# Kernel tuning notes

Measured on AMD Instinct MI355X. Metric: run time of the kernel, lower is better.

Reference implementation:

```python
import jax, jax.numpy as jnp
import numpy as np

N_NODES = 50000
N_EDGES = 800000
HEADS = 5
NFEAT = 5
C1 = 32  # hidden_layers


def setup_inputs() -> dict:
    key = jax.random.key(0)
    ks = jax.random.split(key, 20)
    s = 0.3  # glorot-ish scale
    d = {
        "x": jax.random.normal(ks[0], (N_NODES, NFEAT), jnp.float32),
        "edge_attr": jax.random.uniform(ks[1], (N_EDGES, 1), jnp.float32),
        "src": jax.random.randint(ks[2], (N_EDGES,), 0, N_NODES, jnp.int32),
        "dst": jax.random.randint(ks[3], (N_EDGES,), 0, N_NODES, jnp.int32),
        # conv1: in=5 -> heads=5, out=32, concat
        "W1": jax.random.normal(ks[4], (NFEAT, HEADS * C1), jnp.float32) * s,
        "a_src1": jax.random.normal(ks[5], (HEADS, C1), jnp.float32) * s,
        "a_dst1": jax.random.normal(ks[6], (HEADS, C1), jnp.float32) * s,
        "We1": jax.random.normal(ks[7], (1, HEADS * C1), jnp.float32) * s,
        "ae1": jax.random.normal(ks[8], (HEADS, C1), jnp.float32) * s,
        "b1": jnp.zeros((HEADS * C1,), jnp.float32),
        # conv2: in=160 -> heads=5, out=1, mean over heads
        "W2": jax.random.normal(ks[9], (HEADS * C1, HEADS * 1), jnp.float32) * 0.08,
        "a_src2": jax.random.normal(ks[10], (HEADS, 1), jnp.float32) * s,
        "a_dst2": jax.random.normal(ks[11], (HEADS, 1), jnp.float32) * s,
        "We2": jax.random.normal(ks[12], (1, HEADS * 1), jnp.float32) * s,
        "ae2": jax.random.normal(ks[13], (HEADS, 1), jnp.float32) * s,
        "b2": jnp.zeros((1,), jnp.float32),
        "Wlin": jax.random.normal(ks[14], (1, 1), jnp.float32),
    }
    return d


def gat_layer(x, src, dst, eattr, W, a_src, a_dst, We, a_e, bias, concat, n_nodes):
    """PyG GATConv with edge_dim, self-loops already added by caller."""
    H, C = a_src.shape
    h = (x @ W).reshape(-1, H, C)                      # [N,H,C]
    alpha_s = (h * a_src[None]).sum(-1)                # [N,H]
    alpha_d = (h * a_dst[None]).sum(-1)                # [N,H]
    ee = (eattr @ We).reshape(-1, H, C)                # [E,H,C]
    alpha_e = (ee * a_e[None]).sum(-1)                 # [E,H]
    logits = jax.nn.leaky_relu(alpha_s[src] + alpha_d[dst] + alpha_e, 0.2)
    # segment softmax over destination nodes
    m = jax.ops.segment_max(logits, dst, num_segments=n_nodes)
    m = jnp.where(jnp.isfinite(m), m, 0.0)
    ex = jnp.exp(logits - m[dst])
    denom = jax.ops.segment_sum(ex, dst, num_segments=n_nodes)
    alpha = ex / (denom[dst] + 1e-16)                  # [E,H]
    msg = (alpha[:, :, None] * h[src]).reshape(-1, H * C)
    agg = jax.ops.segment_sum(msg, dst, num_segments=n_nodes).reshape(n_nodes, H, C)
    if concat:
        return agg.reshape(n_nodes, H * C) + bias
    return agg.mean(axis=1) + bias


def reference(x, edge_attr, src, dst, W1, a_src1, a_dst1, We1, ae1, b1,
              W2, a_src2, a_dst2, We2, ae2, b2, Wlin):
    n = x.shape[0]
    loop = jnp.arange(n, dtype=src.dtype)
    s = jnp.concatenate([src, loop])
    t = jnp.concatenate([dst, loop])
    # self-loop edge_attr = mean of edge_attr (PyG fill_value='mean')
    ea_loop = jnp.broadcast_to(edge_attr.mean(axis=0, keepdims=True), (n, edge_attr.shape[1]))
    ea = jnp.concatenate([edge_attr, ea_loop], axis=0)

    x1 = gat_layer(x, s, t, ea, W1, a_src1, a_dst1, We1, ae1, b1, True, n)
    x2 = jax.nn.relu(x1)
    # dropout p=0.2 is identity in eval mode
    x4 = gat_layer(x2, s, t, ea, W2, a_src2, a_dst2, We2, ae2, b2, False, n)
    x5 = x4 @ Wlin                                     # Linear(1,1,bias=False)
    return jax.nn.sigmoid(x5)                          # [N,1]
```

## Files before the change

### kernel.cpp

```cpp
#include <hip/hip_runtime.h>
#include <hip/hip_fp16.h>
#include <math.h>

#define N_NODES 50000
#define N_EDGES 800000
#define E2 (N_EDGES + N_NODES)
#define HEADS 5
#define C1 32
#define F1 160

#define BSZ 64
#define NBK 782
#define NBL 128
#define CH  6641
#define MTOT (NBK*NBL)
#define MC  391
#define GRID_H1 (N_NODES/4)
#define CAP 1408

#define AGG1_NPB 32
#define AGG1_NB  1563

static constexpr size_t alignup(size_t x){ return (x + 255) & ~size_t(255); }
static constexpr size_t OFF_SCAL  = 0;
static constexpr size_t OFF_H     = alignup(OFF_SCAL + 64*4);
static constexpr size_t OFF_EAS   = alignup(OFF_H    + (size_t)MTOT*4);
static constexpr size_t OFF_PART  = alignup(OFF_EAS  + (size_t)NBL*4);
static constexpr size_t OFF_PPREF = alignup(OFF_PART + (size_t)MC*4);
static constexpr size_t OFF_BST   = alignup(OFF_PPREF+ (size_t)MC*4);
static constexpr size_t OFF_OFFS  = alignup(OFF_BST  + (size_t)(NBK+1)*4);
static constexpr size_t OFF_BPACK = alignup(OFF_OFFS + (size_t)(N_NODES+1)*4);
static constexpr size_t OFF_EDG   = alignup(OFF_BPACK+ (size_t)E2*8);
static constexpr size_t OFF_AS16  = alignup(OFF_EDG  + (size_t)E2*4);
static constexpr size_t OFF_AD16  = alignup(OFF_AS16 + (size_t)N_NODES*8*2);
static constexpr size_t OFF_G16   = alignup(OFF_AD16 + (size_t)N_NODES*8*2);
static constexpr size_t OFF_AD2P  = alignup(OFF_G16  + (size_t)N_NODES*16*2);
static constexpr size_t OFF_H1Q   = alignup(OFF_AD2P + (size_t)N_NODES*8*4);
static constexpr size_t OFF_X2H   = alignup(OFF_H1Q  + (size_t)N_NODES*F1);
static constexpr size_t OFF_P2    = alignup(OFF_X2H  + (size_t)N_NODES*F1*2);

typedef float vf2 __attribute__((ext_vector_type(2)));
__device__ __forceinline__ float4 fp8x4_to_f32(unsigned int r){
  vf2 lo = __builtin_amdgcn_cvt_pk_f32_fp8((int)r, false);
  vf2 hi = __builtin_amdgcn_cvt_pk_f32_fp8((int)r, true);
  return make_float4(lo.x, lo.y, hi.x, hi.y);
}

__global__ __launch_bounds__(320) void k_init(const float* __restrict__ x, const float* __restrict__ W1,
                       const float* __restrict__ as1w, const float* __restrict__ ad1w,
                       unsigned short* __restrict__ h1qh, __half* __restrict__ as16, __half* __restrict__ ad16,
                       const int* __restrict__ dst, const float* __restrict__ ea,
                       int* __restrict__ H, float* __restrict__ easum){
  __shared__ float sW[5*F1];
  int t = threadIdx.x;
  if (blockIdx.x < GRID_H1){
    for (int k = t; k < 5*F1; k += 320) sW[k] = W1[k];
    __syncthreads();
    int nl = t / 80;
    int c  = t - nl*80;
    int n  = blockIdx.x*4 + nl;
    int c0 = 2*c;
    float hv0 = 0.f, hv1 = 0.f;
    #pragma unroll
    for (int f = 0; f < 5; f++){
      float xv = x[n*5 + f];
      hv0 += xv * sW[f*F1 + c0];
      hv1 += xv * sW[f*F1 + c0 + 1];
    }
    int pk = __builtin_amdgcn_cvt_pk_fp8_f32(hv0, hv1, 0, false);
    int hh = c >> 4, pp = c & 15;
    h1qh[(size_t)hh*(N_NODES*16) + n*16 + pp] = (unsigned short)(pk & 0xFFFF);
    float vs = hv0*as1w[c0] + hv1*as1w[c0+1];
    float vd = hv0*ad1w[c0] + hv1*ad1w[c0+1];
    #pragma unroll
    for (int m = 8; m >= 1; m >>= 1){
      vs += __shfl_xor(vs, m, 64);
      vd += __shfl_xor(vd, m, 64);
    }
    if ((c & 15) == 0){
      int h = c >> 4;
      as16[n*8 + h] = __float2half(vs);
      ad16[n*8 + h] = __float2half(vd);
    }
  } else {
    int* hist = (int*)sW;
    float* wsum = (float*)&hist[NBK + 1];
    for (int k = t; k < NBK; k += 320) hist[k] = 0;
    __syncthreads();
    int b = blockIdx.x - GRID_H1;
    int e0 = b*CH, e1 = min(e0 + CH, E2);
    float s = 0.f;
    for (int e = e0 + t; e < e1; e += 320){
      int d;
      if (e < N_EDGES){ d = dst[e]; s += ea[e]; }
      else d = e - N_EDGES;
      atomicAdd(&hist[d >> 6], 1);
    }
    #pragma unroll
    for (int m = 1; m < 64; m <<= 1) s += __shfl_xor(s, m, 64);
    if ((t & 63) == 0) wsum[t >> 6] = s;
    __syncthreads();
    for (int k = t; k < NBK; k += 320) H[(size_t)k*NBL + b] = hist[k];
    if (t == 0) easum[b] = wsum[0] + wsum[1] + wsum[2] + wsum[3] + wsum[4];
  }
}

__global__ void k_s1(const int* __restrict__ H, int* __restrict__ partial){
  int i = blockIdx.x*256 + threadIdx.x;
  int v = (i < MTOT) ? H[i] : 0;
  #pragma unroll
  for (int m = 1; m < 64; m <<= 1) v += __shfl_xor(v, m, 64);
  __shared__ int sh[4];
  if ((threadIdx.x & 63) == 0) sh[threadIdx.x >> 6] = v;
  __syncthreads();
  if (threadIdx.x == 0) partial[blockIdx.x] = sh[0] + sh[1] + sh[2] + sh[3];
}

__global__ __launch_bounds__(512) void k_s2p(const int* __restrict__ partial, int* __restrict__ ppref,
                      int* __restrict__ offs, int* __restrict__ bstart,
                      const float* __restrict__ easum,
                      const float* __restrict__ We1, const float* __restrict__ ae1,
                      const float* __restrict__ We2, const float* __restrict__ ae2,
                      float* __restrict__ scal){
  __shared__ int sp[512];
  __shared__ float sh_ea[NBL];
  int t = threadIdx.x;
  if (t < NBL) sh_ea[t] = easum[t];
  if (t >= 448 && t < 448 + HEADS){
    int h = t - 448;
    float s = 0.f;
    for (int c = 0; c < C1; c++) s += We1[h*C1 + c] * ae1[h*C1 + c];
    scal[2 + h] = s;
    scal[7 + h] = We2[h] * ae2[h];
  }
  int v = (t < MC) ? partial[t] : 0;
  sp[t] = v;
  __syncthreads();
  if (t == 511){
    float es = 0.f;
    for (int i = 0; i < NBL; i++) es += sh_ea[i];
    scal[1] = es / (float)N_EDGES;
  }
  for (int off = 1; off < 512; off <<= 1){
    int u = (t >= off) ? sp[t - off] : 0;
    __syncthreads();
    sp[t] += u;
    __syncthreads();
  }
  if (t < MC) ppref[t] = sp[t] - v;
  if (t == 0){ offs[N_NODES] = E2; bstart[NBK] = E2; }
}

__global__ void k_s3(int* __restrict__ H, const int* __restrict__ ppref, int* __restrict__ bstart){
  __shared__ int sp[256];
  int b = blockIdx.x, t = threadIdx.x;
  int i = b*256 + t;
  int v = (i < MTOT) ? H[i] : 0;
  sp[t] = v;
  __syncthreads();
  for (int off = 1; off < 256; off <<= 1){
    int u = (t >= off) ? sp[t - off] : 0;
    __syncthreads();
    sp[t] += u;
    __syncthreads();
  }
  int P = ppref[b] + sp[t] - v;
  if (i < MTOT){
    H[i] = P;
    if (i % NBL == 0) bstart[i / NBL] = P;
  }
}

__global__ __launch_bounds__(256) void k_scat(const int* __restrict__ src, const int* __restrict__ dst,
                       const float* __restrict__ ea, const float* __restrict__ scal,
                       const int* __restrict__ H, int2* __restrict__ bpack){
  __shared__ int lofs[NBK];
  int b = blockIdx.x;
  for (int k = threadIdx.x; k < NBK; k += 256) lofs[k] = H[(size_t)k*NBL + b];
  __syncthreads();
  float mean = scal[1];
  int e0 = b*CH, e1 = min(e0 + CH, E2);
  for (int e = e0 + threadIdx.x; e < e1; e += 256){
    int d, s; float a;
    if (e < N_EDGES){ d = dst[e]; s = src[e]; a = ea[e]; }
    else { d = s = e - N_EDGES; a = mean; }
    int pos = atomicAdd(&lofs[d >> 6], 1);
    bpack[pos] = make_int2(s | ((d & 63) << 16), __float_as_int(a));
  }
}

__global__ __launch_bounds__(256) void k_final2(const int* __restrict__ bstart,
                        const int2* __restrict__ bpack,
                        int* __restrict__ offs, unsigned int* __restrict__ edge2){
  __shared__ int cnt[BSZ], cur[BSZ];
  __shared__ unsigned int s_edge[CAP];
  int k = blockIdx.x, t = threadIdx.x;
  int base = k*BSZ;
  if (t < BSZ) cnt[t] = 0;
  __syncthreads();
  int r0 = bstart[k], r1 = bstart[k + 1];
  int sz = r1 - r0;
  for (int j = r0 + t; j < r1; j += 256) atomicAdd(&cnt[(bpack[j].x >> 16) & 63], 1);
  __syncthreads();
  if (t == 0){
    int run = 0;
    for (int i = 0; i < BSZ; i++){ int c = cnt[i]; cnt[i] = run; cur[i] = run; run += c; }
  }
  __syncthreads();
  if (t < BSZ){
    int n = base + t;
    if (n < N_NODES) offs[n] = r0 + cnt[t];
  }
  if (sz <= CAP){
    for (int j = r0 + t; j < r1; j += 256){
      int2 v = bpack[j];
      int lp = atomicAdd(&cur[(v.x >> 16) & 63], 1);
      s_edge[lp] = (unsigned int)(v.x & 0xFFFF) |
                   ((unsigned int)__half_as_ushort(__float2half(__int_as_float(v.y))) << 16);
    }
    __syncthreads();
    for (int i = t; i < sz; i += 256) edge2[r0 + i] = s_edge[i];
  } else {
    for (int j = r0 + t; j < r1; j += 256){
      int2 v = bpack[j];
      int pos = r0 + atomicAdd(&cur[(v.x >> 16) & 63], 1);
      edge2[pos] = (unsigned int)(v.x & 0xFFFF) |
                   ((unsigned int)__half_as_ushort(__float2half(__int_as_float(v.y))) << 16);
    }
  }
}

__global__ __launch_bounds__(256) void k_logit(const int* __restrict__ offs,
                      const unsigned int* __restrict__ edge2,
                      const __half* __restrict__ as16, const __half* __restrict__ ad16,
                      const float* __restrict__ scal,
                      unsigned int* __restrict__ P01, unsigned int* __restrict__ P2){
  int gl = threadIdx.x >> 3;
  int q  = threadIdx.x & 7;
  int n  = blockIdx.x*AGG1_NPB + gl;
  if (n >= N_NODES) return;
  union { uint4 u; __half2 h[4]; } AD; AD.u = *(const uint4*)(ad16 + (size_t)n*8);
  float ad0 = __low2float(AD.h[0]), ad1 = __high2float(AD.h[0]);
  float ad2 = __low2float(AD.h[1]), ad3 = __high2float(AD.h[1]);
  float ad4 = __low2float(AD.h[2]);
  float wd0 = scal[2], wd1 = scal[3], wd2 = scal[4], wd3 = scal[5], wd4 = scal[6];
  int j0 = offs[n], j1 = offs[n + 1];
  for (int j = j0 + q; j < j1; j += 8){
    unsigned int e = edge2[j];
    unsigned int lo = e & 0xFFFFu;
    int s = (int)lo;
    float c = __half2float(__ushort_as_half((unsigned short)(e >> 16)));
    union { uint4 u; __half2 h[4]; } AS; AS.u = *(const uint4*)(as16 + (size_t)s*8);
    float l0 = __low2float(AS.h[0])  + ad0 + c*wd0;  l0 = fminf(fmaxf(l0, 0.2f*l0), 10.f);
    float l1 = __high2float(AS.h[0]) + ad1 + c*wd1;  l1 = fminf(fmaxf(l1, 0.2f*l1), 10.f);
    float l2 = __low2float(AS.h[1])  + ad2 + c*wd2;  l2 = fminf(fmaxf(l2, 0.2f*l2), 10.f);
    float l3 = __high2float(AS.h[1]) + ad3 + c*wd3;  l3 = fminf(fmaxf(l3, 0.2f*l3), 10.f);
    float l4 = __low2float(AS.h[2])  + ad4 + c*wd4;  l4 = fminf(fmaxf(l4, 0.2f*l4), 10.f);
    unsigned int p0 = (unsigned int)__half_as_ushort(__float2half(__expf(l0)));
    unsigned int p1 = (unsigned int)__half_as_ushort(__float2half(__expf(l1)));
    unsigned int p2 = (unsigned int)__half_as_ushort(__float2half(__expf(l2)));
    unsigned int p3 = (unsigned int)__half_as_ushort(__float2half(__expf(l3)));
    unsigned int p4 = (unsigned int)__half_as_ushort(__float2half(__expf(l4)));
    P01[j]                  = lo | (p0 << 16);
    P01[(size_t)E2 + j]     = lo | (p1 << 16);
    P2[j]                   = lo | (p2 << 16);
    P2[(size_t)E2 + j]      = lo | (p3 << 16);
    P2[(size_t)2*E2 + j]    = lo | (p4 << 16);
  }
}

__global__ __launch_bounds__(256) void k_agg1(const int* __restrict__ offs,
                      const unsigned int* __restrict__ P01, const unsigned int* __restrict__ P2,
                      const unsigned short* __restrict__ h1qh,
                      const float* __restrict__ b1, __half* __restrict__ x2h){
  int head = blockIdx.x / AGG1_NB;
  int nb   = blockIdx.x - head*AGG1_NB;
  int gl   = threadIdx.x >> 3;
  int q    = threadIdx.x & 7;
  int n    = nb*AGG1_NPB + gl;
  if (n >= N_NODES) return;
  const unsigned int* EP = (head < 2) ? (P01 + (size_t)head*E2)
                                      : (P2  + (size_t)(head-2)*E2);
  const unsigned int* h1row = (const unsigned int*)h1qh + (size_t)head*(N_NODES*8) + q;
  int j0 = offs[n], j1 = offs[n + 1];
  float a0 = 0.f, a1 = 0.f, a2 = 0.f, a3 = 0.f, den = 0.f;
  int j = j0;
  for (; j + 7 < j1; j += 8){
    uint4 sa = *(const uint4*)(EP + j);
    uint4 sb = *(const uint4*)(EP + j + 4);
    unsigned int e0 = sa.x, e1 = sa.y, e2v = sa.z, e3 = sa.w;
    unsigned int e4 = sb.x, e5 = sb.y, e6 = sb.z, e7 = sb.w;
    int s0 = e0 & 0xFFFF, s1 = e1 & 0xFFFF, s2 = e2v & 0xFFFF, s3 = e3 & 0xFFFF;
    int s4 = e4 & 0xFFFF, s5 = e5 & 0xFFFF, s6 = e6 & 0xFFFF, s7 = e7 & 0xFFFF;
    unsigned int r0 = h1row[s0*8];
    unsigned int r1 = h1row[s1*8];
    unsigned int r2 = h1row[s2*8];
    unsigned int r3 = h1row[s3*8];
    unsigned int r4 = h1row[s4*8];
    unsigned int r5 = h1row[s5*8];
    unsigned int r6 = h1row[s6*8];
    unsigned int r7 = h1row[s7*8];
    float p0 = __half2float(__ushort_as_half((unsigned short)(e0 >> 16)));
    float p1 = __half2float(__ushort_as_half((unsigned short)(e1 >> 16)));
    float p2 = __half2float(__ushort_as_half((unsigned short)(e2v >> 16)));
    float p3 = __half2float(__ushort_as_half((unsigned short)(e3 >> 16)));
    float p4 = __half2float(__ushort_as_half((unsigned short)(e4 >> 16)));
    float p5 = __half2float(__ushort_as_half((unsigned short)(e5 >> 16)));
    float p6 = __half2float(__ushort_as_half((unsigned short)(e6 >> 16)));
    float p7 = __half2float(__ushort_as_half((unsigned short)(e7 >> 16)));
    den += ((p0 + p1) + (p2 + p3)) + ((p4 + p5) + (p6 + p7));
    float4 f0 = fp8x4_to_f32(r0), f1 = fp8x4_to_f32(r1);
    float4 f2 = fp8x4_to_f32(r2), f3 = fp8x4_to_f32(r3);
    float4 f4 = fp8x4_to_f32(r4), f5 = fp8x4_to_f32(r5);
    float4 f6 = fp8x4_to_f32(r6), f7 = fp8x4_to_f32(r7);
    a0 += p0*f0.x; a1 += p0*f0.y; a2 += p0*f0.z; a3 += p0*f0.w;
    a0 += p1*f1.x; a1 += p1*f1.y; a2 += p1*f1.z; a3 += p1*f1.w;
    a0 += p2*f2.x; a1 += p2*f2.y; a2 += p2*f2.z; a3 += p2*f2.w;
    a0 += p3*f3.x; a1 += p3*f3.y; a2 += p3*f3.z; a3 += p3*f3.w;
    a0 += p4*f4.x; a1 += p4*f4.y; a2 += p4*f4.z; a3 += p4*f4.w;
    a0 += p5*f5.x; a1 += p5*f5.y; a2 += p5*f5.z; a3 += p5*f5.w;
    a0 += p6*f6.x; a1 += p6*f6.y; a2 += p6*f6.z; a3 += p6*f6.w;
    a0 += p7*f7.x; a1 += p7*f7.y; a2 += p7*f7.z; a3 += p7*f7.w;
  }
  for (; j < j1; ++j){
    unsigned int e = EP[j];
    int s = e & 0xFFFF;
    float p = __half2float(__ushort_as_half((unsigned short)(e >> 16)));
    den += p;
    float4 f = fp8x4_to_f32(h1row[s*8]);
    a0 += p*f.x; a1 += p*f.y; a2 += p*f.z; a3 += p*f.w;
  }
  float inv = 1.f / (den + 1e-16f);
  float4 bb = *(const float4*)(b1 + head*C1 + 4*q);
  float v0 = fmaxf(a0*inv + bb.x, 0.f);
  float v1 = fmaxf(a1*inv + bb.y, 0.f);
  float v2 = fmaxf(a2*inv + bb.z, 0.f);
  float v3 = fmaxf(a3*inv + bb.w, 0.f);
  __half2 o0 = __floats2half2_rn(v0, v1);
  __half2 o1 = __floats2half2_rn(v2, v3);
  *(uint2*)(x2h + (size_t)n*F1 + head*C1 + 4*q) =
      make_uint2(*(unsigned int*)&o0, *(unsigned int*)&o1);
}

__global__ __launch_bounds__(256) void k_h2(const __half* __restrict__ x2h, const float* __restrict__ W2,
                    const float* __restrict__ asw2, const float* __restrict__ adw2,
                    __half* __restrict__ G16, float* __restrict__ ad2p){
  __shared__ float sW[F1*HEADS];
  for (int k = threadIdx.x; k < F1*HEADS; k += 256) sW[k] = W2[k];
  __syncthreads();
  int w = threadIdx.x >> 6, l = threadIdx.x & 63;
  int n = blockIdx.x*4 + w;
  const __half2* x22 = (const __half2*)x2h;
  float acc[HEADS] = {0.f, 0.f, 0.f, 0.f, 0.f};
  for (int k2 = l; k2 < 80; k2 += 64){
    float2 f = __half22float2(x22[(size_t)n*80 + k2]);
    #pragma unroll
    for (int h = 0; h < HEADS; h++)
      acc[h] += f.x * sW[(2*k2)*HEADS + h] + f.y * sW[(2*k2+1)*HEADS + h];
  }
  #pragma unroll
  for (int m = 1; m < 64; m <<= 1){
    #pragma unroll
    for (int h = 0; h < HEADS; h++) acc[h] += __shfl_xor(acc[h], m, 64);
  }
  if (l == 0){
    #pragma unroll
    for (int h = 0; h < HEADS; h++){
      G16[(size_t)n*16 + h]     = __float2half(acc[h]);
      G16[(size_t)n*16 + 5 + h] = __float2half(acc[h] * asw2[h]);
      ad2p[n*8 + h]             = acc[h] * adw2[h];
    }
    #pragma unroll
    for (int z = 10; z < 16; z++) G16[(size_t)n*16 + z] = __float2half(0.f);
  }
}

__global__ __launch_bounds__(256) void k_agg2(const int* __restrict__ offs,
                      const unsigned int* __restrict__ edge2,
                      const __half* __restrict__ G16, const float* __restrict__ ad2p,
                      const float* __restrict__ scal,
                      const float* __restrict__ b2, const float* __restrict__ Wlin,
                      float* __restrict__ out){
  int grp = threadIdx.x >> 4;
  int l16 = threadIdx.x & 15;
  int n = blockIdx.x*16 + grp;
  float adn[HEADS], wd[HEADS];
  #pragma unroll
  for (int h = 0; h < HEADS; h++){ adn[h] = ad2p[n*8 + h]; wd[h] = scal[7 + h]; }
  int j0 = offs[n], j1 = offs[n + 1];

  float den[HEADS] = {0,0,0,0,0};
  float ac[HEADS]  = {0,0,0,0,0};
  for (int j = j0 + l16; j < j1; j += 16){
    unsigned int e = edge2[j];
    int s = e & 0xFFFF;
    float c = __half2float(__ushort_as_half((unsigned short)(e >> 16)));
    const __half* gs = G16 + (size_t)s*16;
    union { uint4 u; __half2 h[4]; } U; U.u = *(const uint4*)gs;
    union { uint2 u; __half2 h[2]; } V; V.u = *(const uint2*)(gs + 8);
    float2 p01 = __half22float2(U.h[0]);
    float2 p23 = __half22float2(U.h[1]);
    float2 p45 = __half22float2(U.h[2]);
    float2 p67 = __half22float2(U.h[3]);
    float2 p89 = __half22float2(V.h[0]);
    float hv[HEADS] = {p01.x, p01.y, p23.x, p23.y, p45.x};
    float av[HEADS] = {p45.y, p67.x, p67.y, p89.x, p89.y};
    #pragma unroll
    for (int h = 0; h < HEADS; h++){
      float lg = av[h] + adn[h] + c*wd[h];
      lg = fmaxf(lg, 0.2f*lg);
      lg = fminf(lg, 50.f);
      float p = __expf(lg);
      den[h] += p;
      ac[h]  += p * hv[h];
    }
  }
  #pragma unroll
  for (int m = 1; m < 16; m <<= 1){
    #pragma unroll
    for (int h = 0; h < HEADS; h++){
      den[h] += __shfl_xor(den[h], m, 16);
      ac[h]  += __shfl_xor(ac[h], m, 16);
    }
  }
  if (l16 == 0){
    float v = 0.f;
    #pragma unroll
    for (int h = 0; h < HEADS; h++) v += ac[h] / (den[h] + 1e-16f);
    v = v * (1.f/HEADS) + b2[0];
    v *= Wlin[0];
    out[n] = 1.f / (1.f + __expf(-v));
  }
}

extern "C" void kernel_launch(void* const* d_in, const int* in_sizes, int n_in,
                              void* d_out, int out_size, void* d_ws, size_t ws_size,
                              hipStream_t stream) {
  const float* x    = (const float*)d_in[0];
  const float* ea   = (const float*)d_in[1];
  const int*   src  = (const int*)d_in[2];
  const int*   dst  = (const int*)d_in[3];
  const float* W1   = (const float*)d_in[4];
  const float* as1w = (const float*)d_in[5];
  const float* ad1w = (const float*)d_in[6];
  const float* We1  = (const float*)d_in[7];
  const float* ae1  = (const float*)d_in[8];
  const float* b1   = (const float*)d_in[9];
  const float* W2   = (const float*)d_in[10];
  const float* as2w = (const float*)d_in[11];
  const float* ad2w = (const float*)d_in[12];
  const float* We2  = (const float*)d_in[13];
  const float* ae2  = (const float*)d_in[14];
  const float* b2   = (const float*)d_in[15];
  const float* Wlin = (const float*)d_in[16];

  char* ws = (char*)d_ws;
  float* scal   = (float*)(ws + OFF_SCAL);
  int*   H      = (int*)  (ws + OFF_H);
  float* easum  = (float*)(ws + OFF_EAS);
  int*   part   = (int*)  (ws + OFF_PART);
  int*   ppref  = (int*)  (ws + OFF_PPREF);
  int*   bstart = (int*)  (ws + OFF_BST);
  int*   offs   = (int*)  (ws + OFF_OFFS);
  int2*  bpack  = (int2*) (ws + OFF_BPACK);
  unsigned int* P01 = (unsigned int*)(ws + OFF_BPACK);
  unsigned int* P2  = (unsigned int*)(ws + OFF_P2);
  unsigned int* edge2 = (unsigned int*)(ws + OFF_EDG);
  __half* as16  = (__half*)(ws + OFF_AS16);
  __half* ad16  = (__half*)(ws + OFF_AD16);
  __half* G16   = (__half*)(ws + OFF_G16);
  float* ad2p   = (float*)(ws + OFF_AD2P);
  unsigned short* h1qh = (unsigned short*)(ws + OFF_H1Q);
  __half* x2h   = (__half*)(ws + OFF_X2H);
  float* outp   = (float*)d_out;

  k_init   <<<GRID_H1 + NBL, 320, 0, stream>>>(x, W1, as1w, ad1w, h1qh, as16, ad16,
                                               dst, ea, H, easum);
  k_s1     <<<MC, 256, 0, stream>>>(H, part);
  k_s2p    <<<1, 512, 0, stream>>>(part, ppref, offs, bstart, easum, We1, ae1, We2, ae2, scal);
  k_s3     <<<MC, 256, 0, stream>>>(H, ppref, bstart);
  k_scat   <<<NBL, 256, 0, stream>>>(src, dst, ea, scal, H, bpack);
  k_final2 <<<NBK, 256, 0, stream>>>(bstart, bpack, offs, edge2);

  k_logit  <<<AGG1_NB, 256, 0, stream>>>(offs, edge2, as16, ad16, scal, P01, P2);
  k_agg1   <<<HEADS*AGG1_NB, 256, 0, stream>>>(offs, P01, P2, h1qh, b1, x2h);
  k_h2     <<<N_NODES/4, 256, 0, stream>>>(x2h, W2, as2w, ad2w, G16, ad2p);
  k_agg2   <<<N_NODES/16, 256, 0, stream>>>(offs, edge2, G16, ad2p, scal, b2, Wlin, outp);
}
```

Before: 224.1 us.

## Replace bucketed CSR build with per-node atomic scatter and fuse W2 into agg1

The two-level bucket histogram, scan and local sort used to build the CSR are replaced by a per-node degree count with global atomics, a flat scan, and a scatter that claims slots through per-node cursor atomics. The layer-2 linear projection is folded into the layer-1 aggregation epilogue as per-head partial sums, which a small kernel then adds together, so the fp16 x2 intermediate and its reread are dropped. The G16 record shrinks to 8 halves, and the source attention term is recomputed in agg2 instead of being stored. The edge order inside each node now depends on atomic timing, and contention on global atomics may cost more than the shared-memory buckets did.

```diff
diff --git a/kernel.cpp b/kernel.cpp
--- a/kernel.cpp
+++ b/kernel.cpp
@@ -9,35 +9,31 @@
 #define C1 32
 #define F1 160
 
-#define BSZ 64
-#define NBK 782
 #define NBL 128
 #define CH  6641
-#define MTOT (NBK*NBL)
-#define MC  391
 #define GRID_H1 (N_NODES/4)
-#define CAP 1408
+#define SC_NB 196
 
 #define AGG1_NPB 32
 #define AGG1_NB  1563
 
 static constexpr size_t alignup(size_t x){ return (x + 255) & ~size_t(255); }
 static constexpr size_t OFF_SCAL  = 0;
-static constexpr size_t OFF_H     = alignup(OFF_SCAL + 64*4);
-static constexpr size_t OFF_EAS   = alignup(OFF_H    + (size_t)MTOT*4);
+static constexpr size_t OFF_DEG   = alignup(OFF_SCAL + 64*4);
+static constexpr size_t OFF_CUR   = alignup(OFF_DEG  + (size_t)N_NODES*4);
+static constexpr size_t OFF_EAS   = alignup(OFF_CUR  + (size_t)N_NODES*4);
 static constexpr size_t OFF_PART  = alignup(OFF_EAS  + (size_t)NBL*4);
-static constexpr size_t OFF_PPREF = alignup(OFF_PART + (size_t)MC*4);
-static constexpr size_t OFF_BST   = alignup(OFF_PPREF+ (size_t)MC*4);
-static constexpr size_t OFF_OFFS  = alignup(OFF_BST  + (size_t)(NBK+1)*4);
-static constexpr size_t OFF_BPACK = alignup(OFF_OFFS + (size_t)(N_NODES+1)*4);
-static constexpr size_t OFF_EDG   = alignup(OFF_BPACK+ (size_t)E2*8);
+static constexpr size_t OFF_PPREF = alignup(OFF_PART + (size_t)SC_NB*4);
+static constexpr size_t OFF_OFFS  = alignup(OFF_PPREF+ (size_t)256*4);
+static constexpr size_t OFF_EDG   = alignup(OFF_OFFS + (size_t)(N_NODES+1)*4);
 static constexpr size_t OFF_AS16  = alignup(OFF_EDG  + (size_t)E2*4);
 static constexpr size_t OFF_AD16  = alignup(OFF_AS16 + (size_t)N_NODES*8*2);
 static constexpr size_t OFF_G16   = alignup(OFF_AD16 + (size_t)N_NODES*8*2);
-static constexpr size_t OFF_AD2P  = alignup(OFF_G16  + (size_t)N_NODES*16*2);
+static constexpr size_t OFF_AD2P  = alignup(OFF_G16  + (size_t)N_NODES*8*2);
 static constexpr size_t OFF_H1Q   = alignup(OFF_AD2P + (size_t)N_NODES*8*4);
-static constexpr size_t OFF_X2H   = alignup(OFF_H1Q  + (size_t)N_NODES*F1);
-static constexpr size_t OFF_P2    = alignup(OFF_X2H  + (size_t)N_NODES*F1*2);
+static constexpr size_t OFF_P01   = alignup(OFF_H1Q  + (size_t)N_NODES*F1);
+static constexpr size_t OFF_P2    = alignup(OFF_P01  + (size_t)2*E2*4);
+static constexpr size_t OFF_H2P   = alignup(OFF_P2   + (size_t)3*E2*4);
 
 typedef float vf2 __attribute__((ext_vector_type(2)));
 __device__ __forceinline__ float4 fp8x4_to_f32(unsigned int r){
@@ -46,11 +42,16 @@
   return make_float4(lo.x, lo.y, hi.x, hi.y);
 }
 
+__global__ __launch_bounds__(256) void k_zero(int* __restrict__ deg){
+  int i = blockIdx.x*256 + threadIdx.x;
+  if (i < N_NODES) deg[i] = 0;
+}
+
 __global__ __launch_bounds__(320) void k_init(const float* __restrict__ x, const float* __restrict__ W1,
                        const float* __restrict__ as1w, const float* __restrict__ ad1w,
                        unsigned short* __restrict__ h1qh, __half* __restrict__ as16, __half* __restrict__ ad16,
                        const int* __restrict__ dst, const float* __restrict__ ea,
-                       int* __restrict__ H, float* __restrict__ easum){
+                       int* __restrict__ deg, float* __restrict__ easum){
   __shared__ float sW[5*F1];
   int t = threadIdx.x;
   if (blockIdx.x < GRID_H1){
@@ -83,10 +84,7 @@
       ad16[n*8 + h] = __float2half(vd);
     }
   } else {
-    int* hist = (int*)sW;
-    float* wsum = (float*)&hist[NBK + 1];
-    for (int k = t; k < NBK; k += 320) hist[k] = 0;
-    __syncthreads();
+    float* wsum = (float*)sW;
     int b = blockIdx.x - GRID_H1;
     int e0 = b*CH, e1 = min(e0 + CH, E2);
     float s = 0.f;
@@ -94,68 +92,67 @@
       int d;
       if (e < N_EDGES){ d = dst[e]; s += ea[e]; }
       else d = e - N_EDGES;
-      atomicAdd(&hist[d >> 6], 1);
+      atomicAdd(&deg[d], 1);
     }
     #pragma unroll
     for (int m = 1; m < 64; m <<= 1) s += __shfl_xor(s, m, 64);
     if ((t & 63) == 0) wsum[t >> 6] = s;
     __syncthreads();
-    for (int k = t; k < NBK; k += 320) H[(size_t)k*NBL + b] = hist[k];
     if (t == 0) easum[b] = wsum[0] + wsum[1] + wsum[2] + wsum[3] + wsum[4];
   }
 }
 
-__global__ void k_s1(const int* __restrict__ H, int* __restrict__ partial){
+__global__ __launch_bounds__(256) void k_scanA(const int* __restrict__ deg, int* __restrict__ part){
   int i = blockIdx.x*256 + threadIdx.x;
-  int v = (i < MTOT) ? H[i] : 0;
+  int v = (i < N_NODES) ? deg[i] : 0;
   #pragma unroll
   for (int m = 1; m < 64; m <<= 1) v += __shfl_xor(v, m, 64);
   __shared__ int sh[4];
   if ((threadIdx.x & 63) == 0) sh[threadIdx.x >> 6] = v;
   __syncthreads();
-  if (threadIdx.x == 0) partial[blockIdx.x] = sh[0] + sh[1] + sh[2] + sh[3];
-}
-
-__global__ __launch_bounds__(512) void k_s2p(const int* __restrict__ partial, int* __restrict__ ppref,
-                      int* __restrict__ offs, int* __restrict__ bstart,
-                      const float* __restrict__ easum,
+  if (threadIdx.x == 0) part[blockIdx.x] = sh[0] + sh[1] + sh[2] + sh[3];
+}
+
+__global__ __launch_bounds__(256) void k_scanB(const int* __restrict__ part, int* __restrict__ ppref,
+                      int* __restrict__ offs, const float* __restrict__ easum,
                       const float* __restrict__ We1, const float* __restrict__ ae1,
                       const float* __restrict__ We2, const float* __restrict__ ae2,
                       float* __restrict__ scal){
-  __shared__ int sp[512];
+  __shared__ int sp[256];
   __shared__ float sh_ea[NBL];
   int t = threadIdx.x;
   if (t < NBL) sh_ea[t] = easum[t];
-  if (t >= 448 && t < 448 + HEADS){
-    int h = t - 448;
+  if (t >= 200 && t < 200 + HEADS){
+    int h = t - 200;
     float s = 0.f;
     for (int c = 0; c < C1; c++) s += We1[h*C1 + c] * ae1[h*C1 + c];
     scal[2 + h] = s;
     scal[7 + h] = We2[h] * ae2[h];
   }
-  int v = (t < MC) ? partial[t] : 0;
+  int v = (t < SC_NB) ? part[t] : 0;
   sp[t] = v;
   __syncthreads();
-  if (t == 511){
+  if (t == 255){
     float es = 0.f;
     for (int i = 0; i < NBL; i++) es += sh_ea[i];
     scal[1] = es / (float)N_EDGES;
   }
-  for (int off = 1; off < 512; off <<= 1){
+  for (int off = 1; off < 256; off <<= 1){
     int u = (t >= off) ? sp[t - off] : 0;
     __syncthreads();
     sp[t] += u;
     __syncthreads();
   }
-  if (t < MC) ppref[t] = sp[t] - v;
-  if (t == 0){ offs[N_NODES] = E2; bstart[NBK] = E2; }
-}
-
-__global__ void k_s3(int* __restrict__ H, const int* __restrict__ ppref, int* __restrict__ bstart){
+  if (t < SC_NB) ppref[t] = sp[t] - v;
+  if (t == 0) offs[N_NODES] = E2;
+}
+
+__global__ __launch_bounds__(256) void k_scanC(const int* __restrict__ deg, const int* __restrict__ ppref,
+                      int* __restrict__ offs, int* __restrict__ cursor){
   __shared__ int sp[256];
   int b = blockIdx.x, t = threadIdx.x;
   int i = b*256 + t;
-  int v = (i < MTOT) ? H[i] : 0;
+  int v = (i < N_NODES) ? deg[i] : 0;
   sp[t] = v;
   __syncthreads();
   for (int off = 1; off < 256; off <<= 1){
@@ -165,72 +162,24 @@
     __syncthreads();
   }
   int P = ppref[b] + sp[t] - v;
-  if (i < MTOT){
-    H[i] = P;
-    if (i % NBL == 0) bstart[i / NBL] = P;
-  }
-}
-
-__global__ __launch_bounds__(256) void k_scat(const int* __restrict__ src, const int* __restrict__ dst,
+  if (i < N_NODES){ offs[i] = P; cursor[i] = P; }
+}
+
+__global__ __launch_bounds__(256) void k_scat2(const int* __restrict__ src, const int* __restrict__ dst,
                        const float* __restrict__ ea, const float* __restrict__ scal,
-                       const int* __restrict__ H, int2* __restrict__ bpack){
-  __shared__ int lofs[NBK];
-  int b = blockIdx.x;
-  for (int k = threadIdx.x; k < NBK; k += 256) lofs[k] = H[(size_t)k*NBL + b];
-  __syncthreads();
+                       int* __restrict__ cursor, unsigned int* __restrict__ edge2){
+  int e = blockIdx.x*256 + threadIdx.x;
+  if (e >= E2) return;
   float mean = scal[1];
-  int e0 = b*CH, e1 = min(e0 + CH, E2);
-  for (int e = e0 + threadIdx.x; e < e1; e += 256){
-    int d, s; float a;
-    if (e < N_EDGES){ d = dst[e]; s = src[e]; a = ea[e]; }
-    else { d = s = e - N_EDGES; a = mean; }
-    int pos = atomicAdd(&lofs[d >> 6], 1);
-    bpack[pos] = make_int2(s | ((d & 63) << 16), __float_as_int(a));
-  }
-}
-
-__global__ __launch_bounds__(256) void k_final2(const int* __restrict__ bstart,
-                        const int2* __restrict__ bpack,
-                        int* __restrict__ offs, unsigned int* __restrict__ edge2){
-  __shared__ int cnt[BSZ], cur[BSZ];
-  __shared__ unsigned int s_edge[CAP];
-  int k = blockIdx.x, t = threadIdx.x;
-  int base = k*BSZ;
-  if (t < BSZ) cnt[t] = 0;
-  __syncthreads();
-  int r0 = bstart[k], r1 = bstart[k + 1];
-  int sz = r1 - r0;
-  for (int j = r0 + t; j < r1; j += 256) atomicAdd(&cnt[(bpack[j].x >> 16) & 63], 1);
-  __syncthreads();
-  if (t == 0){
-    int run = 0;
-    for (int i = 0; i < BSZ; i++){ int c = cnt[i]; cnt[i] = run; cur[i] = run; run += c; }
-  }
-  __syncthreads();
-  if (t < BSZ){
-    int n = base + t;
-    if (n < N_NODES) offs[n] = r0 + cnt[t];
-  }
-  if (sz <= CAP){
-    for (int j = r0 + t; j < r1; j += 256){
-      int2 v = bpack[j];
-      int lp = atomicAdd(&cur[(v.x >> 16) & 63], 1);
-      s_edge[lp] = (unsigned int)(v.x & 0xFFFF) |
-                   ((unsigned int)__half_as_ushort(__float2half(__int_as_float(v.y))) << 16);
-    }
-    __syncthreads();
-    for (int i = t; i < sz; i += 256) edge2[r0 + i] = s_edge[i];
-  } else {
-    for (int j = r0 + t; j < r1; j += 256){
-      int2 v = bpack[j];
-      int pos = r0 + atomicAdd(&cur[(v.x >> 16) & 63], 1);
-      edge2[pos] = (unsigned int)(v.x & 0xFFFF) |
-                   ((unsigned int)__half_as_ushort(__float2half(__int_as_float(v.y))) << 16);
-    }
-  }
-}
-
-__global__ __launch_bounds__(256) void k_logit(const int* __restrict__ offs,
+  int d, s; float a;
+  if (e < N_EDGES){ d = dst[e]; s = src[e]; a = ea[e]; }
+  else { d = s = e - N_EDGES; a = mean; }
+  int pos = atomicAdd(&cursor[d], 1);
+  edge2[pos] = (unsigned int)s |
+               ((unsigned int)__half_as_ushort(__float2half(a)) << 16);
+}
+
+__global__ __launch_bounds__(256) void k_ep(const int* __restrict__ offs,
                       const unsigned int* __restrict__ edge2,
                       const __half* __restrict__ as16, const __half* __restrict__ ad16,
                       const float* __restrict__ scal,
@@ -256,25 +205,24 @@
     float l2 = __low2float(AS.h[1])  + ad2 + c*wd2;  l2 = fminf(fmaxf(l2, 0.2f*l2), 10.f);
     float l3 = __high2float(AS.h[1]) + ad3 + c*wd3;  l3 = fminf(fmaxf(l3, 0.2f*l3), 10.f);
     float l4 = __low2float(AS.h[2])  + ad4 + c*wd4;  l4 = fminf(fmaxf(l4, 0.2f*l4), 10.f);
-    unsigned int p0 = (unsigned int)__half_as_ushort(__float2half(__expf(l0)));
-    unsigned int p1 = (unsigned int)__half_as_ushort(__float2half(__expf(l1)));
-    unsigned int p2 = (unsigned int)__half_as_ushort(__float2half(__expf(l2)));
-    unsigned int p3 = (unsigned int)__half_as_ushort(__float2half(__expf(l3)));
-    unsigned int p4 = (unsigned int)__half_as_ushort(__float2half(__expf(l4)));
-    P01[j]                  = lo | (p0 << 16);
-    P01[(size_t)E2 + j]     = lo | (p1 << 16);
-    P2[j]                   = lo | (p2 << 16);
-    P2[(size_t)E2 + j]      = lo | (p3 << 16);
-    P2[(size_t)2*E2 + j]    = lo | (p4 << 16);
+    P01[j]                = lo | ((unsigned int)__half_as_ushort(__float2half(__expf(l0))) << 16);
+    P01[(size_t)E2 + j]   = lo | ((unsigned int)__half_as_ushort(__float2half(__expf(l1))) << 16);
+    P2[j]                 = lo | ((unsigned int)__half_as_ushort(__float2half(__expf(l2))) << 16);
+    P2[(size_t)E2 + j]    = lo | ((unsigned int)__half_as_ushort(__float2half(__expf(l3))) << 16);
+    P2[(size_t)2*E2 + j]  = lo | ((unsigned int)__half_as_ushort(__float2half(__expf(l4))) << 16);
   }
 }
 
 __global__ __launch_bounds__(256) void k_agg1(const int* __restrict__ offs,
                       const unsigned int* __restrict__ P01, const unsigned int* __restrict__ P2,
                       const unsigned short* __restrict__ h1qh,
-                      const float* __restrict__ b1, __half* __restrict__ x2h){
+                      const float* __restrict__ b1, const float* __restrict__ W2,
+                      float* __restrict__ h2part){
   int head = blockIdx.x / AGG1_NB;
   int nb   = blockIdx.x - head*AGG1_NB;
+  __shared__ float sW2[C1*HEADS];
+  for (int i = threadIdx.x; i < C1*HEADS; i += 256) sW2[i] = W2[head*C1*HEADS + i];
+  __syncthreads();
   int gl   = threadIdx.x >> 3;
   int q    = threadIdx.x & 7;
   int n    = nb*AGG1_NPB + gl;
@@ -336,57 +284,60 @@
   float v1 = fmaxf(a1*inv + bb.y, 0.f);
   float v2 = fmaxf(a2*inv + bb.z, 0.f);
   float v3 = fmaxf(a3*inv + bb.w, 0.f);
-  __half2 o0 = __floats2half2_rn(v0, v1);
-  __half2 o1 = __floats2half2_rn(v2, v3);
-  *(uint2*)(x2h + (size_t)n*F1 + head*C1 + 4*q) =
-      make_uint2(*(unsigned int*)&o0, *(unsigned int*)&o1);
-}
-
-__global__ __launch_bounds__(256) void k_h2(const __half* __restrict__ x2h, const float* __restrict__ W2,
-                    const float* __restrict__ asw2, const float* __restrict__ adw2,
+  const float* wr = sW2 + (4*q)*HEADS;
+  float hh[HEADS];
+  #pragma unroll
+  for (int h2i = 0; h2i < HEADS; h2i++)
+    hh[h2i] = v0*wr[0*HEADS + h2i] + v1*wr[1*HEADS + h2i]
+            + v2*wr[2*HEADS + h2i] + v3*wr[3*HEADS + h2i];
+  #pragma unroll
+  for (int m = 1; m < 8; m <<= 1){
+    #pragma unroll
+    for (int h2i = 0; h2i < HEADS; h2i++) hh[h2i] += __shfl_xor(hh[h2i], m, 8);
+  }
+  if (q == 0){
+    float* hp = h2part + ((size_t)head*N_NODES + n)*HEADS;
+    hp[0] = hh[0]; hp[1] = hh[1]; hp[2] = hh[2]; hp[3] = hh[3]; hp[4] = hh[4];
+  }
+}
+
+__global__ __launch_bounds__(256) void k_h2b(const float* __restrict__ h2part,
+                    const float* __restrict__ adw2,
                     __half* __restrict__ G16, float* __restrict__ ad2p){
-  __shared__ float sW[F1*HEADS];
-  for (int k = threadIdx.x; k < F1*HEADS; k += 256) sW[k] = W2[k];
-  __syncthreads();
-  int w = threadIdx.x >> 6, l = threadIdx.x & 63;
-  int n = blockIdx.x*4 + w;
-  const __half2* x22 = (const __half2*)x2h;
-  float acc[HEADS] = {0.f, 0.f, 0.f, 0.f, 0.f};
-  for (int k2 = l; k2 < 80; k2 += 64){
-    float2 f = __half22float2(x22[(size_t)n*80 + k2]);
-    #pragma unroll
-    for (int h = 0; h < HEADS; h++)
-      acc[h] += f.x * sW[(2*k2)*HEADS + h] + f.y * sW[(2*k2+1)*HEADS + h];
-  }
-  #pragma unroll
-  for (int m = 1; m < 64; m <<= 1){
-    #pragma unroll
-    for (int h = 0; h < HEADS; h++) acc[h] += __shfl_xor(acc[h], m, 64);
-  }
-  if (l == 0){
-    #pragma unroll
-    for (int h = 0; h < HEADS; h++){
-      G16[(size_t)n*16 + h]     = __float2half(acc[h]);
-      G16[(size_t)n*16 + 5 + h] = __float2half(acc[h] * asw2[h]);
-      ad2p[n*8 + h]             = acc[h] * adw2[h];
-    }
-    #pragma unroll
-    for (int z = 10; z < 16; z++) G16[(size_t)n*16 + z] = __float2half(0.f);
-  }
+  int n = blockIdx.x*256 + threadIdx.x;
+  if (n >= N_NODES) return;
+  float a0 = 0.f, a1 = 0.f, a2 = 0.f, a3 = 0.f, a4 = 0.f;
+  #pragma unroll
+  for (int hd = 0; hd < HEADS; hd++){
+    const float* hp = h2part + ((size_t)hd*N_NODES + n)*HEADS;
+    a0 += hp[0]; a1 += hp[1]; a2 += hp[2]; a3 += hp[3]; a4 += hp[4];
+  }
+  __half2 g0 = __floats2half2_rn(a0, a1);
+  __half2 g1 = __floats2half2_rn(a2, a3);
+  __half2 g2 = __floats2half2_rn(a4, 0.f);
+  __half2 g3 = __floats2half2_rn(0.f, 0.f);
+  *(uint4*)(G16 + (size_t)n*8) = make_uint4(*(unsigned int*)&g0, *(unsigned int*)&g1,
+                                            *(unsigned int*)&g2, *(unsigned int*)&g3);
+  float4 d0 = make_float4(a0*adw2[0], a1*adw2[1], a2*adw2[2], a3*adw2[3]);
+  float4 d1 = make_float4(a4*adw2[4], 0.f, 0.f, 0.f);
+  *(float4*)(ad2p + (size_t)n*8)     = d0;
+  *(float4*)(ad2p + (size_t)n*8 + 4) = d1;
 }
 
 __global__ __launch_bounds__(256) void k_agg2(const int* __restrict__ offs,
                       const unsigned int* __restrict__ edge2,
                       const __half* __restrict__ G16, const float* __restrict__ ad2p,
-                      const float* __restrict__ scal,
+                      const float* __restrict__ scal, const float* __restrict__ asw2,
                       const float* __restrict__ b2, const float* __restrict__ Wlin,
                       float* __restrict__ out){
   int grp = threadIdx.x >> 4;
   int l16 = threadIdx.x & 15;
   int n = blockIdx.x*16 + grp;
-  float adn[HEADS], wd[HEADS];
-  #pragma unroll
-  for (int h = 0; h < HEADS; h++){ adn[h] = ad2p[n*8 + h]; wd[h] = scal[7 + h]; }
+  float adn[HEADS], wd[HEADS], asw[HEADS];
+  #pragma unroll
+  for (int h = 0; h < HEADS; h++){
+    adn[h] = ad2p[n*8 + h]; wd[h] = scal[7 + h]; asw[h] = asw2[h];
+  }
   int j0 = offs[n], j1 = offs[n + 1];
 
   float den[HEADS] = {0,0,0,0,0};
@@ -395,19 +346,14 @@
     unsigned int e = edge2[j];
     int s = e & 0xFFFF;
     float c = __half2float(__ushort_as_half((unsigned short)(e >> 16)));
-    const __half* gs = G16 + (size_t)s*16;
-    union { uint4 u; __half2 h[4]; } U; U.u = *(const uint4*)gs;
-    union { uint2 u; __half2 h[2]; } V; V.u = *(const uint2*)(gs + 8);
+    union { uint4 u; __half2 h[4]; } U; U.u = *(const uint4*)(G16 + (size_t)s*8);
     float2 p01 = __half22float2(U.h[0]);
     float2 p23 = __half22float2(U.h[1]);
     float2 p45 = __half22float2(U.h[2]);
-    float2 p67 = __half22float2(U.h[3]);
-    float2 p89 = __half22float2(V.h[0]);
     float hv[HEADS] = {p01.x, p01.y, p23.x, p23.y, p45.x};
-    float av[HEADS] = {p45.y, p67.x, p67.y, p89.x, p89.y};
     #pragma unroll
     for (int h = 0; h < HEADS; h++){
-      float lg = av[h] + adn[h] + c*wd[h];
+      float lg = hv[h]*asw[h] + adn[h] + c*wd[h];
       lg = fmaxf(lg, 0.2f*lg);
       lg = fminf(lg, 50.f);
       float p = __expf(lg);
@@ -456,34 +402,33 @@
 
   char* ws = (char*)d_ws;
   float* scal   = (float*)(ws + OFF_SCAL);
-  int*   H      = (int*)  (ws + OFF_H);
+  int*   deg    = (int*)  (ws + OFF_DEG);
+  int*   cursor = (int*)  (ws + OFF_CUR);
   float* easum  = (float*)(ws + OFF_EAS);
   int*   part   = (int*)  (ws + OFF_PART);
   int*   ppref  = (int*)  (ws + OFF_PPREF);
-  int*   bstart = (int*)  (ws + OFF_BST);
   int*   offs   = (int*)  (ws + OFF_OFFS);
-  int2*  bpack  = (int2*) (ws + OFF_BPACK);
-  unsigned int* P01 = (unsigned int*)(ws + OFF_BPACK);
+  unsigned int* edge2 = (unsigned int*)(ws + OFF_EDG);
+  unsigned int* P01 = (unsigned int*)(ws + OFF_P01);
   unsigned int* P2  = (unsigned int*)(ws + OFF_P2);
-  unsigned int* edge2 = (unsigned int*)(ws + OFF_EDG);
   __half* as16  = (__half*)(ws + OFF_AS16);
   __half* ad16  = (__half*)(ws + OFF_AD16);
   __half* G16   = (__half*)(ws + OFF_G16);
   float* ad2p   = (float*)(ws + OFF_AD2P);
   unsigned short* h1qh = (unsigned short*)(ws + OFF_H1Q);
-  __half* x2h   = (__half*)(ws + OFF_X2H);
+  float* h2part = (float*)(ws + OFF_H2P);
   float* outp   = (float*)d_out;
 
-  k_init   <<<GRID_H1 + NBL, 320, 0, stream>>>(x, W1, as1w, ad1w, h1qh, as16, ad16,
-                                               dst, ea, H, easum);
-  k_s1     <<<MC, 256, 0, stream>>>(H, part);
-  k_s2p    <<<1, 512, 0, stream>>>(part, ppref, offs, bstart, easum, We1, ae1, We2, ae2, scal);
-  k_s3     <<<MC, 256, 0, stream>>>(H, ppref, bstart);
-  k_scat   <<<NBL, 256, 0, stream>>>(src, dst, ea, scal, H, bpack);
-  k_final2 <<<NBK, 256, 0, stream>>>(bstart, bpack, offs, edge2);
-
-  k_logit  <<<AGG1_NB, 256, 0, stream>>>(offs, edge2, as16, ad16, scal, P01, P2);
-  k_agg1   <<<HEADS*AGG1_NB, 256, 0, stream>>>(offs, P01, P2, h1qh, b1, x2h);
-  k_h2     <<<N_NODES/4, 256, 0, stream>>>(x2h, W2, as2w, ad2w, G16, ad2p);
-  k_agg2   <<<N_NODES/16, 256, 0, stream>>>(offs, edge2, G16, ad2p, scal, b2, Wlin, outp);
-}
+  k_zero  <<<SC_NB, 256, 0, stream>>>(deg);
+  k_init  <<<GRID_H1 + NBL, 320, 0, stream>>>(x, W1, as1w, ad1w, h1qh, as16, ad16,
+                                              dst, ea, deg, easum);
+  k_scanA <<<SC_NB, 256, 0, stream>>>(deg, part);
+  k_scanB <<<1, 256, 0, stream>>>(part, ppref, offs, easum, We1, ae1, We2, ae2, scal);
+  k_scanC <<<SC_NB, 256, 0, stream>>>(deg, ppref, offs, cursor);
+  k_scat2 <<<(E2 + 255)/256, 256, 0, stream>>>(src, dst, ea, scal, cursor, edge2);
+  k_ep    <<<AGG1_NB, 256, 0, stream>>>(offs, edge2, as16, ad16, scal, P01, P2);
+
+  k_agg1  <<<HEADS*AGG1_NB, 256, 0, stream>>>(offs, P01, P2, h1qh, b1, W2, h2part);
+  k_h2b   <<<SC_NB, 256, 0, stream>>>(h2part, ad2w, G16, ad2p);
+  k_agg2  <<<N_NODES/16, 256, 0, stream>>>(offs, edge2, G16, ad2p, scal, as2w, b2, Wlin, outp);
+}
```

Result: slower. 273.6 us (+22.1%).
